# Kernel optimization log

Measured on AMD Instinct MI355X. Metric: run time of the kernel, lower is better.

## Reference

```python
import jax, jax.numpy as jnp
import numpy as np

D = 64      # feature_dim / hidden dim
L = 4       # conv layers per sub-net (len(hidden_dims))
B = 4       # query batch
N = 20000   # entity nodes
R = 256     # relation-graph nodes (= relations)
E = 300000  # entity-graph edges
ER = 40000  # edges per relation-graph direction (hh/ht/th/tt)
NNEG = 32   # candidate relations per query


def _mlp2(x, W1, b1, W2, b2):
    # Linear -> ReLU -> Linear (used for relation_projection and the 2-layer MLPs)
    return jnp.maximum(x @ W1 + b1, 0.0) @ W2 + b2


def _conv(x, boundary, rel_raw, src, dst, etype, num_nodes, W1, b1, W2, b2, Wl, bl):
    # GeneralizedRelationalConv: project relations, distmult message, sum-aggregate
    # with boundary self-loop, then linear(cat[input, agg]) + ReLU.
    rel = _mlp2(rel_raw, W1, b1, W2, b2)            # (B, R, D) relation_projection
    msg = x[:, src, :] * rel[:, etype, :]            # (B, E, D) distmult message
    agg = jax.vmap(lambda m: jax.ops.segment_sum(m, dst, num_segments=num_nodes))(msg)
    agg = agg + boundary                             # self-loop carries boundary
    out = jnp.concatenate([x, agg], axis=-1) @ Wl + bl
    return jax.nn.relu(out)


def setup_inputs() -> dict:
    key = jax.random.key(0)
    ks = jax.random.split(key, 32)
    p = lambda k, shape: jax.random.normal(k, shape, jnp.float32) * 0.05
    h = jax.random.randint(ks[0], (B,), 0, N)
    t = jax.random.randint(ks[1], (B,), 0, N)
    r = jax.random.randint(ks[2], (B, NNEG), 0, R // 2)
    batch = jnp.stack([jnp.broadcast_to(h[:, None], (B, NNEG)),
                       jnp.broadcast_to(t[:, None], (B, NNEG)), r], axis=-1)
    return {
        'batch': batch,
        'ent_edge_index': jax.random.randint(ks[3], (2, E), 0, N),
        'ent_edge_type': jax.random.randint(ks[4], (E,), 0, R),
        'rel_edge_index': jax.random.randint(ks[5], (4, 2, ER), 0, R),
        'rel_edge_type': jax.random.randint(ks[6], (4, ER), 0, N),
        'num_nodes': N,
        'num_rel_nodes': R,
        'ent_W1': p(ks[7], (L, D, D)), 'ent_b1': p(ks[8], (L, D)),
        'ent_W2': p(ks[9], (L, D, D)), 'ent_b2': p(ks[10], (L, D)),
        'ent_Wl': p(ks[11], (L, 2 * D, D)), 'ent_bl': p(ks[12], (L, D)),
        'rel_W1': p(ks[13], (4, L, D, D)), 'rel_b1': p(ks[14], (4, L, D)),
        'rel_W2': p(ks[15], (4, L, D, D)), 'rel_b2': p(ks[16], (4, L, D)),
        'rel_Wl': p(ks[17], (4, L, 2 * D, D)), 'rel_bl': p(ks[18], (4, L, D)),
        'ent_mlp_W1': p(ks[19], (2 * D, 2 * D)), 'ent_mlp_b1': p(ks[20], (2 * D,)),
        'ent_mlp_W2': p(ks[21], (2 * D, D)), 'ent_mlp_b2': p(ks[22], (D,)),
        'trix_W1': p(ks[23], (D, D)), 'trix_b1': p(ks[24], (D,)),
        'trix_W2': p(ks[25], (D, 1)), 'trix_b2': p(ks[26], (1,)),
    }


def reference(batch, ent_edge_index, ent_edge_type, rel_edge_index, rel_edge_type,
              num_nodes, num_rel_nodes,
              ent_W1, ent_b1, ent_W2, ent_b2, ent_Wl, ent_bl,
              rel_W1, rel_b1, rel_W2, rel_b2, rel_Wl, rel_bl,
              ent_mlp_W1, ent_mlp_b1, ent_mlp_W2, ent_mlp_b2,
              trix_W1, trix_b1, trix_W2, trix_b2):
    Bq = batch.shape[0]
    h, t, r = batch[:, 0, 0], batch[:, 0, 1], batch[:, :, 2]
    ar = jnp.arange(Bq)
    query = jnp.ones((Bq, D), jnp.float32)  # relation_representations start as ones
    node_reps = jnp.zeros((Bq, num_nodes, D), jnp.float32)
    node_reps = node_reps.at[ar, h].add(query).at[ar, t].add(-query)
    rel_reps = jnp.ones((Bq, num_rel_nodes, D), jnp.float32)
    esrc, edst = ent_edge_index[0], ent_edge_index[1]

    # --- TRIX block (num_layer = 1): EntityNet then RelNet ---
    # EntityNet bellman-ford over entity graph
    boundary = jnp.zeros((Bq, num_nodes, D), jnp.float32)
    boundary = boundary.at[ar, h].add(query).at[ar, t].add(-query)
    x = node_reps
    for l in range(L):
        hid = _conv(x, boundary, rel_reps, esrc, edst, ent_edge_type, num_nodes,
                    ent_W1[l], ent_b1[l], ent_W2[l], ent_b2[l], ent_Wl[l], ent_bl[l])
        x = hid + x  # short_cut
    node_query = jnp.broadcast_to(query[:, None, :], (Bq, num_nodes, D))
    feat = jnp.concatenate([x, node_query], axis=-1)  # (B, N, 2D)
    node_reps = _mlp2(feat, ent_mlp_W1, ent_mlp_b1, ent_mlp_W2, ent_mlp_b2)

    # RelNet over 4 relation-graph directions
    boundary_r = jnp.ones((Bq, num_rel_nodes, D), jnp.float32)
    y = rel_reps
    for l in range(L):
        hid = jnp.zeros_like(y)
        for d in range(4):
            hid = hid + _conv(y, boundary_r, node_reps,
                              rel_edge_index[d, 0], rel_edge_index[d, 1], rel_edge_type[d],
                              num_rel_nodes,
                              rel_W1[d, l], rel_b1[d, l], rel_W2[d, l], rel_b2[d, l],
                              rel_Wl[d, l], rel_bl[d, l])
        y = hid + y  # short_cut
    rel_reps = y

    feat = rel_reps[ar[:, None], r]  # gather candidate relation features (B, NNEG, D)
    score = _mlp2(feat, trix_W1, trix_b1, trix_W2, trix_b2)[..., 0]
    return score
```

## Files before the change

kernel.cpp:

```cpp
#include <hip/hip_runtime.h>

typedef long long i64;
#define CDIV(a,b) (((a)+(b)-1)/(b))

#define NN   20000
#define RRN  256
#define BB   4
#define LLAY 4

__global__ void k_fill2i(int* p1, int n1, int* p2, int n2){
  int i=blockIdx.x*256+threadIdx.x;
  if(i<n1) p1[i]=0;
  if(i<n2) p2[i]=0;
}

__global__ void k_hist_ent(const int* __restrict__ dst, int* __restrict__ cnt, int E){
  int e=blockIdx.x*256+threadIdx.x; if(e<E) atomicAdd(&cnt[dst[e]],1);
}
__global__ void k_scan_ent(int* cnt_cur, int* rp, int n){
  __shared__ int sm[1024];
  __shared__ int carry;
  int tx=threadIdx.x;
  if(tx==0) carry=0;
  __syncthreads();
  for(int base=0;base<n;base+=1024){
    int i=base+tx;
    int val=(i<n)?cnt_cur[i]:0;
    sm[tx]=val; __syncthreads();
    for(int off=1;off<1024;off<<=1){
      int t=(tx>=off)?sm[tx-off]:0; __syncthreads();
      sm[tx]+=t; __syncthreads();
    }
    int excl=carry+sm[tx]-val;
    if(i<n){ rp[i]=excl; cnt_cur[i]=excl; }
    __syncthreads();
    if(tx==0) carry+=sm[1023];
    __syncthreads();
  }
  if(tx==0) rp[n]=carry;
}
__global__ void k_fill_ent(const int* __restrict__ src, const int* __restrict__ dst,
                           int* __restrict__ cur, int* __restrict__ colsrc, int E){
  int e=blockIdx.x*256+threadIdx.x;
  if(e<E){ int p=atomicAdd(&cur[dst[e]],1); colsrc[p]=src[e]; }
}

__global__ void k_hist_rel(const int* __restrict__ rei, int* __restrict__ cnt, int ER){
  int e=blockIdx.x*256+threadIdx.x; int d=blockIdx.y;
  if(e<ER) atomicAdd(&cnt[d*256 + rei[(i64)(2*d+1)*ER + e]],1);
}
__global__ void k_scan_rel(int* cnt_cur, int* rp){
  __shared__ int sm[256];
  int d=blockIdx.x, tx=threadIdx.x;
  int val=cnt_cur[d*256+tx];
  sm[tx]=val; __syncthreads();
  for(int off=1;off<256;off<<=1){
    int t=(tx>=off)?sm[tx-off]:0; __syncthreads();
    sm[tx]+=t; __syncthreads();
  }
  int excl=sm[tx]-val;
  rp[d*257+tx]=excl;
  cnt_cur[d*256+tx]=excl;
  if(tx==255) rp[d*257+256]=sm[255];
}
__global__ void k_fill_rel(const int* __restrict__ rei, int* __restrict__ cur,
                           int* __restrict__ colr, int ER){
  int e=blockIdx.x*256+threadIdx.x; int d=blockIdx.y;
  if(e<ER){
    int dst=rei[(i64)(2*d+1)*ER+e];
    int p=atomicAdd(&cur[d*256+dst],1);
    colr[d*ER+p]=e;
  }
}

__global__ void k_init_x(float* __restrict__ x, const int* __restrict__ batch, int N){
  int i=blockIdx.x*256+threadIdx.x;
  int total=N*64;
  if(i>=total) return;
  int n=i>>6; int b=(i>>4)&3;
  int h=batch[b*96], t=batch[b*96+1];
  float bnd=(n==h?1.f:0.f)-(n==t?1.f:0.f);
  ((float4*)x)[i]=make_float4(bnd,bnd,bnd,bnd);
}

__global__ void k_ventity_all(const float* __restrict__ W1, const float* __restrict__ b1,
                              const float* __restrict__ W2, const float* __restrict__ b2,
                              float* __restrict__ v){
  __shared__ float sh[64];
  int l=blockIdx.x;
  const float* W1l=W1+(i64)l*4096;
  const float* W2l=W2+(i64)l*4096;
  int j=threadIdx.x;
  float s=b1[l*64+j];
  for(int i=0;i<64;i++) s+=W1l[i*64+j];
  sh[j]=fmaxf(s,0.f);
  __syncthreads();
  float vd=b2[l*64+j];
  for(int k=0;k<64;k++) vd+=sh[k]*W2l[k*64+j];
  v[l*64+j]=vd;
}

__global__ void k_badj(const float* __restrict__ W1, const float* __restrict__ b1,
                       float* __restrict__ badj){
  int j=threadIdx.x;
  float s=b1[j];
  for(int k=0;k<64;k++) s+=W1[(64+k)*128+j];
  badj[j]=s;
}

__global__ __launch_bounds__(256) void k_spmm_ent(
    const float* __restrict__ x, const float* __restrict__ v,
    const int* __restrict__ rp, const int* __restrict__ col,
    const int* __restrict__ batch, float* __restrict__ agg, int N){
  int gw=blockIdx.x*4+(threadIdx.x>>6);
  int lane=threadIdx.x&63;
  if(gw>=N) return;
  int n=gw;
  int beg=rp[n], end=rp[n+1];
  float a0=0.f,a1=0.f,a2=0.f,a3=0.f;
  int e=beg;
  for(; e+2<=end; e+=2){
    int s0=col[e], s1=col[e+1];
    const float* r0=x+(i64)s0*256;
    const float* r1=x+(i64)s1*256;
    a0+=r0[lane];     a1+=r0[64+lane];
    a2+=r0[128+lane]; a3+=r0[192+lane];
    a0+=r1[lane];     a1+=r1[64+lane];
    a2+=r1[128+lane]; a3+=r1[192+lane];
  }
  if(e<end){
    const float* r0=x+(i64)col[e]*256;
    a0+=r0[lane]; a1+=r0[64+lane]; a2+=r0[128+lane]; a3+=r0[192+lane];
  }
  float vl=v[lane];
  #pragma unroll
  for(int b=0;b<4;b++){
    int h=batch[b*96], t=batch[b*96+1];
    float bnd=(n==h?1.f:0.f)-(n==t?1.f:0.f);
    float av=(b==0)?a0:(b==1)?a1:(b==2)?a2:a3;
    agg[((i64)n*4+b)*64+lane]=av*vl+bnd;
  }
}

__global__ __launch_bounds__(256) void k_spmm_rel(
    const float* __restrict__ y, const float* __restrict__ relbuf, i64 rbs,
    const int* __restrict__ rp_rel, const int* __restrict__ col_rel,
    const int* __restrict__ rei, const int* __restrict__ ret,
    float* __restrict__ aggr, int d0, int ER){
  __shared__ float s_acc[4][4][64];
  int rr=blockIdx.x; int ch=blockIdx.y; int dz=blockIdx.z;
  int d=d0+dz;
  const float* rb=relbuf+(i64)dz*rbs;
  int tx=threadIdx.x; int ws=tx>>6; int lane=tx&63;
  int beg=rp_rel[d*257+rr], end=rp_rel[d*257+rr+1];
  int len=end-beg;
  int per=(len+3)>>2;
  int cb=beg+ch*per;
  int ce_=cb+per; if(ce_>end) ce_=end;
  int clen=ce_-cb; if(clen<0) clen=0;
  int perw=(clen+3)>>2;
  int e0=cb+ws*perw;
  int e1=e0+perw; if(e1>ce_) e1=ce_;
  const int* cidx=col_rel+(i64)d*ER;
  const int* srcA=rei+(i64)(2*d)*ER;
  const int* etA=ret+(i64)d*ER;
  float a0=0.f,a1=0.f,a2=0.f,a3=0.f;
  for(int e=e0;e<e1;++e){
    int eid=cidx[e];
    int s=srcA[eid], t=etA[eid];
    const float* yr=y+(i64)s*64;
    const float* rr2=rb+(i64)t*256;
    a0+=yr[0*16384+lane]*rr2[     lane];
    a1+=yr[1*16384+lane]*rr2[ 64+lane];
    a2+=yr[2*16384+lane]*rr2[128+lane];
    a3+=yr[3*16384+lane]*rr2[192+lane];
  }
  s_acc[ws][0][lane]=a0; s_acc[ws][1][lane]=a1;
  s_acc[ws][2][lane]=a2; s_acc[ws][3][lane]=a3;
  __syncthreads();
  int b=ws;
  float vv=s_acc[0][b][lane]+s_acc[1][b][lane]+s_acc[2][b][lane]+s_acc[3][b][lane];
  atomicAdd(&aggr[((i64)(d*4+b)*256+rr)*64+lane],vv);
}

template<int KC, bool RELU, int OP>
__global__ __launch_bounds__(256,4) void k_gemm64(
    const float* __restrict__ inA, int lda,
    const float* __restrict__ inB, int ldb, i64 inBs,
    const float* __restrict__ W, int ldw, i64 Ws,
    const float* __restrict__ bias, i64 biasS,
    float* out, int ldo, i64 outS,
    const float* resid, int ldr,
    int rows){
  __shared__ float s_in[128*68];
  __shared__ float s_wt[64*68];
  int tx=threadIdx.x;
  int dy=blockIdx.y;
  const float* Wd=W+(i64)dy*Ws;
  const float* biasd=bias+(i64)dy*biasS;
  float* outd=out+(i64)dy*outS;
  int row0=blockIdx.x*128;
  int rslot=tx>>4, c0=tx&15;
  float acc[8][4];
  #pragma unroll
  for(int j=0;j<8;j++)
    #pragma unroll
    for(int cc=0;cc<4;cc++) acc[j][cc]=0.f;
  for(int kc=0;kc<KC;++kc){
    const float* in=(kc==0)?inA:(inB+(i64)dy*inBs);
    int ld=(kc==0)?lda:ldb;
    #pragma unroll
    for(int i=0;i<8;i++){
      int id=i*256+tx;
      int r=id>>4, k4=id&15;
      int gr=row0+r;
      float4 val=make_float4(0.f,0.f,0.f,0.f);
      if(gr<rows) val=*(const float4*)(in+(i64)gr*ld+k4*4);
      *(float4*)&s_in[r*68+k4*4]=val;
    }
    #pragma unroll
    for(int i=0;i<4;i++){
      int id=i*256+tx;
      int k=id>>4, c4=(id&15)*4;
      float4 wv=*(const float4*)(Wd+(i64)(kc*64+k)*ldw+c4);
      s_wt[(c4+0)*68+k]=wv.x; s_wt[(c4+1)*68+k]=wv.y;
      s_wt[(c4+2)*68+k]=wv.z; s_wt[(c4+3)*68+k]=wv.w;
    }
    __syncthreads();
    #pragma unroll 4
    for(int k4=0;k4<16;k4++){
      float4 wv[4];
      #pragma unroll
      for(int cc=0;cc<4;cc++) wv[cc]=*(const float4*)&s_wt[(c0+16*cc)*68+k4*4];
      #pragma unroll
      for(int j=0;j<8;j++){
        float4 iv=*(const float4*)&s_in[(rslot+16*j)*68+k4*4];
        #pragma unroll
        for(int cc=0;cc<4;cc++)
          acc[j][cc]+=iv.x*wv[cc].x+iv.y*wv[cc].y+iv.z*wv[cc].z+iv.w*wv[cc].w;
      }
    }
    __syncthreads();
  }
  #pragma unroll
  for(int j=0;j<8;j++){
    int r=row0+rslot+16*j;
    if(r>=rows) continue;
    #pragma unroll
    for(int cc=0;cc<4;cc++){
      int c=c0+16*cc;
      float vv=acc[j][cc]+biasd[c];
      if(RELU) vv=fmaxf(vv,0.f);
      if(OP==1) vv+=resid[(i64)r*ldr+c];
      outd[(i64)r*ldo+c]=vv;
    }
  }
}

__global__ __launch_bounds__(256,4) void k_mlp128(
    const float* __restrict__ in,
    const float* __restrict__ W1, i64 w1s,
    const float* __restrict__ b1, i64 b1s,
    const float* __restrict__ W2, i64 w2s,
    const float* __restrict__ b2, i64 b2s,
    float* __restrict__ out, i64 outs,
    int rows){
  __shared__ float s_in[128*68];
  __shared__ float s_wt[64*68];
  int tx=threadIdx.x;
  int dy=blockIdx.y;
  const float* W1d=W1+(i64)dy*w1s;
  const float* b1d=b1+(i64)dy*b1s;
  const float* W2d=W2+(i64)dy*w2s;
  const float* b2d=b2+(i64)dy*b2s;
  float* outd=out+(i64)dy*outs;
  int row0=blockIdx.x*128;
  int rslot=tx>>4, c0=tx&15;
  #pragma unroll
  for(int i=0;i<8;i++){
    int id=i*256+tx;
    int r=id>>4, k4=id&15;
    int gr=row0+r;
    float4 val=make_float4(0.f,0.f,0.f,0.f);
    if(gr<rows) val=*(const float4*)(in+(i64)gr*64+k4*4);
    *(float4*)&s_in[r*68+k4*4]=val;
  }
  #pragma unroll
  for(int i=0;i<4;i++){
    int id=i*256+tx;
    int k=id>>4, c4=(id&15)*4;
    float4 wv=*(const float4*)(W1d+(i64)k*64+c4);
    s_wt[(c4+0)*68+k]=wv.x; s_wt[(c4+1)*68+k]=wv.y;
    s_wt[(c4+2)*68+k]=wv.z; s_wt[(c4+3)*68+k]=wv.w;
  }
  __syncthreads();
  float acc[8][4];
  #pragma unroll
  for(int j=0;j<8;j++)
    #pragma unroll
    for(int cc=0;cc<4;cc++) acc[j][cc]=0.f;
  #pragma unroll 4
  for(int k4=0;k4<16;k4++){
    float4 wv[4];
    #pragma unroll
    for(int cc=0;cc<4;cc++) wv[cc]=*(const float4*)&s_wt[(c0+16*cc)*68+k4*4];
    #pragma unroll
    for(int j=0;j<8;j++){
      float4 iv=*(const float4*)&s_in[(rslot+16*j)*68+k4*4];
      #pragma unroll
      for(int cc=0;cc<4;cc++)
        acc[j][cc]+=iv.x*wv[cc].x+iv.y*wv[cc].y+iv.z*wv[cc].z+iv.w*wv[cc].w;
    }
  }
  __syncthreads();
  #pragma unroll
  for(int j=0;j<8;j++)
    #pragma unroll
    for(int cc=0;cc<4;cc++)
      s_in[(rslot+16*j)*68+(c0+16*cc)]=fmaxf(acc[j][cc]+b1d[c0+16*cc],0.f);
  #pragma unroll
  for(int i=0;i<4;i++){
    int id=i*256+tx;
    int k=id>>4, c4=(id&15)*4;
    float4 wv=*(const float4*)(W2d+(i64)k*64+c4);
    s_wt[(c4+0)*68+k]=wv.x; s_wt[(c4+1)*68+k]=wv.y;
    s_wt[(c4+2)*68+k]=wv.z; s_wt[(c4+3)*68+k]=wv.w;
  }
  __syncthreads();
  #pragma unroll
  for(int j=0;j<8;j++)
    #pragma unroll
    for(int cc=0;cc<4;cc++) acc[j][cc]=0.f;
  #pragma unroll 4
  for(int k4=0;k4<16;k4++){
    float4 wv[4];
    #pragma unroll
    for(int cc=0;cc<4;cc++) wv[cc]=*(const float4*)&s_wt[(c0+16*cc)*68+k4*4];
    #pragma unroll
    for(int j=0;j<8;j++){
      float4 iv=*(const float4*)&s_in[(rslot+16*j)*68+k4*4];
      #pragma unroll
      for(int cc=0;cc<4;cc++)
        acc[j][cc]+=iv.x*wv[cc].x+iv.y*wv[cc].y+iv.z*wv[cc].z+iv.w*wv[cc].w;
    }
  }
  #pragma unroll
  for(int j=0;j<8;j++){
    int r=row0+rslot+16*j;
    if(r>=rows) continue;
    #pragma unroll
    for(int cc=0;cc<4;cc++)
      outd[(i64)r*64+c0+16*cc]=acc[j][cc]+b2d[c0+16*cc];
  }
}

__global__ __launch_bounds__(256,4) void k_mlp_ent(
    float* __restrict__ x,
    const float* __restrict__ W1,
    const float* __restrict__ badj,
    const float* __restrict__ W2,
    const float* __restrict__ b2o,
    int rows){
  __shared__ float s_in[64*68];
  __shared__ float s_h[64*68];
  __shared__ float s_wt[64*68];
  int tx=threadIdx.x;
  int row0=blockIdx.x*64;
  int rslot=tx>>4, c0=tx&15;
  #pragma unroll
  for(int i=0;i<4;i++){
    int id=i*256+tx;
    int r=id>>4, k4=id&15;
    int gr=row0+r;
    float4 val=make_float4(0.f,0.f,0.f,0.f);
    if(gr<rows) val=*(const float4*)(x+(i64)gr*64+k4*4);
    *(float4*)&s_in[r*68+k4*4]=val;
  }
  float accO[4][4];
  #pragma unroll
  for(int j=0;j<4;j++)
    #pragma unroll
    for(int cc=0;cc<4;cc++) accO[j][cc]=0.f;
  for(int half=0;half<2;++half){
    __syncthreads();
    #pragma unroll
    for(int i=0;i<4;i++){
      int id=i*256+tx;
      int k=id>>4, c4=(id&15)*4;
      float4 wv=*(const float4*)(W1+(i64)k*128+half*64+c4);
      s_wt[(c4+0)*68+k]=wv.x; s_wt[(c4+1)*68+k]=wv.y;
      s_wt[(c4+2)*68+k]=wv.z; s_wt[(c4+3)*68+k]=wv.w;
    }
    __syncthreads();
    float acc[4][4];
    #pragma unroll
    for(int j=0;j<4;j++)
      #pragma unroll
      for(int cc=0;cc<4;cc++) acc[j][cc]=0.f;
    #pragma unroll 4
    for(int k4=0;k4<16;k4++){
      float4 wv[4];
      #pragma unroll
      for(int cc=0;cc<4;cc++) wv[cc]=*(const float4*)&s_wt[(c0+16*cc)*68+k4*4];
      #pragma unroll
      for(int j=0;j<4;j++){
        float4 iv=*(const float4*)&s_in[(rslot+16*j)*68+k4*4];
        #pragma unroll
        for(int cc=0;cc<4;cc++)
          acc[j][cc]+=iv.x*wv[cc].x+iv.y*wv[cc].y+iv.z*wv[cc].z+iv.w*wv[cc].w;
      }
    }
    __syncthreads();
    #pragma unroll
    for(int j=0;j<4;j++)
      #pragma unroll
      for(int cc=0;cc<4;cc++)
        s_h[(rslot+16*j)*68+(c0+16*cc)]=fmaxf(acc[j][cc]+badj[half*64+c0+16*cc],0.f);
    #pragma unroll
    for(int i=0;i<4;i++){
      int id=i*256+tx;
      int k=id>>4, c4=(id&15)*4;
      float4 wv=*(const float4*)(W2+(i64)(half*64+k)*64+c4);
      s_wt[(c4+0)*68+k]=wv.x; s_wt[(c4+1)*68+k]=wv.y;
      s_wt[(c4+2)*68+k]=wv.z; s_wt[(c4+3)*68+k]=wv.w;
    }
    __syncthreads();
    #pragma unroll 4
    for(int k4=0;k4<16;k4++){
      float4 wv[4];
      #pragma unroll
      for(int cc=0;cc<4;cc++) wv[cc]=*(const float4*)&s_wt[(c0+16*cc)*68+k4*4];
      #pragma unroll
      for(int j=0;j<4;j++){
        float4 iv=*(const float4*)&s_h[(rslot+16*j)*68+k4*4];
        #pragma unroll
        for(int cc=0;cc<4;cc++)
          accO[j][cc]+=iv.x*wv[cc].x+iv.y*wv[cc].y+iv.z*wv[cc].z+iv.w*wv[cc].w;
      }
    }
  }
  #pragma unroll
  for(int j=0;j<4;j++){
    int r=row0+rslot+16*j;
    if(r>=rows) continue;
    #pragma unroll
    for(int cc=0;cc<4;cc++)
      x[(i64)r*64+c0+16*cc]=accO[j][cc]+b2o[c0+16*cc];
  }
}

__global__ void k_yupd_fill(float* __restrict__ y, const float* __restrict__ h,
                            float* __restrict__ aggr){
  int i=blockIdx.x*256+threadIdx.x;
  if(i<65536) y[i]+=h[i]+h[65536+i]+h[131072+i]+h[196608+i];
  if(i<262144) aggr[i]=1.0f;
}

__global__ void k_init_rel(float* __restrict__ y, float* __restrict__ aggr){
  int i=blockIdx.x*256+threadIdx.x;
  if(i<65536) y[i]=1.0f;
  if(i<262144) aggr[i]=1.0f;
}

__global__ __launch_bounds__(256) void k_trix(
    const float* __restrict__ y, const int* __restrict__ batch,
    const float* __restrict__ W1, const float* __restrict__ b1,
    const float* __restrict__ W2, const float* __restrict__ b2,
    float* __restrict__ out){
  __shared__ float s_w1[64*65];
  int tx=threadIdx.x;
  for(int i=tx;i<4096;i+=256){
    int k=i>>6, j=i&63;
    s_w1[k*65+j]=W1[i];
  }
  __syncthreads();
  int wave=tx>>6, lane=tx&63;
  for(int row=wave;row<128;row+=4){
    int b=row>>5, i=row&31;
    int ridx=batch[b*96+i*3+2];
    const float* f=y+((i64)b*256+ridx)*64;
    float hj=b1[lane];
    for(int k=0;k<64;k++) hj+=f[k]*s_w1[k*65+lane];
    hj=fmaxf(hj,0.f);
    float contrib=hj*W2[lane];
    for(int off=32;off;off>>=1) contrib+=__shfl_down(contrib,off);
    if(lane==0) out[row]=contrib+b2[0];
  }
}

extern "C" void kernel_launch(void* const* d_in, const int* in_sizes, int n_in,
                              void* d_out, int out_size, void* d_ws, size_t ws_size,
                              hipStream_t stream){
  const int* batch=(const int*)d_in[0];
  const int* eei  =(const int*)d_in[1];
  const int* rei  =(const int*)d_in[3];
  const int* ret  =(const int*)d_in[4];
  const float* entW1=(const float*)d_in[7];
  const float* entb1=(const float*)d_in[8];
  const float* entW2=(const float*)d_in[9];
  const float* entb2=(const float*)d_in[10];
  const float* entWl=(const float*)d_in[11];
  const float* entbl=(const float*)d_in[12];
  const float* relW1=(const float*)d_in[13];
  const float* relb1=(const float*)d_in[14];
  const float* relW2=(const float*)d_in[15];
  const float* relb2=(const float*)d_in[16];
  const float* relWl=(const float*)d_in[17];
  const float* relbl=(const float*)d_in[18];
  const float* mW1=(const float*)d_in[19];
  const float* mb1=(const float*)d_in[20];
  const float* mW2=(const float*)d_in[21];
  const float* mb2=(const float*)d_in[22];
  const float* tW1=(const float*)d_in[23];
  const float* tb1=(const float*)d_in[24];
  const float* tW2=(const float*)d_in[25];
  const float* tb2=(const float*)d_in[26];
  const int E =in_sizes[2];
  const int ER=in_sizes[4]/4;
  float* out=(float*)d_out;

  float* ws=(float*)d_ws;
  float* x     =ws;
  float* buf   =x+5120000;
  float* aggr  =buf+5120000;
  float* hidr  =aggr+262144;
  float* y     =hidr+262144;
  float* v     =y+65536;
  float* badj  =v+256;
  int* rp_ent =(int*)(badj+128);
  int* cur_ent=rp_ent+NN+1;
  int* col_ent=cur_ent+NN;
  int* rp_rel =col_ent+E;
  int* cur_rel=rp_rel+4*257;
  int* col_rel=cur_rel+1024;
  size_t buf2_off=((size_t)(col_rel+4*ER-(int*)d_ws)+3)&~(size_t)3;
  float* buf2 =(float*)d_ws+buf2_off;

  size_t needed =(buf2_off)*4;
  size_t needed2=(buf2_off+(size_t)5120000)*4;
  if(ws_size<needed) return;
  const bool two=(ws_size>=needed2);
  const i64 bufStride=(i64)(buf2-buf);

  const int* esrc=eei;
  const int* edst=eei+E;

  k_fill2i<<<CDIV(NN,256),256,0,stream>>>(cur_ent,NN,cur_rel,1024);
  k_hist_ent<<<CDIV(E,256),256,0,stream>>>(edst,cur_ent,E);
  k_scan_ent<<<1,1024,0,stream>>>(cur_ent,rp_ent,NN);
  k_fill_ent<<<CDIV(E,256),256,0,stream>>>(esrc,edst,cur_ent,col_ent,E);
  k_hist_rel<<<dim3(CDIV(ER,256),4),256,0,stream>>>(rei,cur_rel,ER);
  k_scan_rel<<<4,256,0,stream>>>(cur_rel,rp_rel);
  k_fill_rel<<<dim3(CDIV(ER,256),4),256,0,stream>>>(rei,cur_rel,col_rel,ER);

  k_ventity_all<<<LLAY,64,0,stream>>>(entW1,entb1,entW2,entb2,v);
  k_badj<<<1,128,0,stream>>>(mW1,mb1,badj);

  k_init_x<<<CDIV(NN*64,256),256,0,stream>>>(x,batch,NN);
  for(int l=0;l<LLAY;l++){
    k_spmm_ent<<<CDIV(NN,4),256,0,stream>>>(x,v+(i64)l*64,rp_ent,col_ent,batch,buf,NN);
    k_gemm64<2,true,1><<<625,256,0,stream>>>(x,64, buf,64,0,
        entWl+(i64)l*8192,64,0, entbl+(i64)l*64,0, x,64,0, x,64, 80000);
  }
  k_mlp_ent<<<1250,256,0,stream>>>(x,mW1,badj,mW2,mb2,80000);

  k_init_rel<<<1024,256,0,stream>>>(y,aggr);
  for(int l=0;l<LLAY;l++){
    if(two){
      for(int d=0;d<4;d+=2){
        k_mlp128<<<dim3(625,2),256,0,stream>>>(x,
            relW1+(i64)(d*LLAY+l)*4096,(i64)LLAY*4096,
            relb1+(i64)(d*LLAY+l)*64,(i64)LLAY*64,
            relW2+(i64)(d*LLAY+l)*4096,(i64)LLAY*4096,
            relb2+(i64)(d*LLAY+l)*64,(i64)LLAY*64,
            buf,bufStride, 80000);
        k_spmm_rel<<<dim3(256,4,2),256,0,stream>>>(y,buf,bufStride,
            rp_rel,col_rel,rei,ret,aggr,d,ER);
      }
    } else {
      for(int d=0;d<4;d++){
        k_mlp128<<<dim3(625,1),256,0,stream>>>(x,
            relW1+(i64)(d*LLAY+l)*4096,0,
            relb1+(i64)(d*LLAY+l)*64,0,
            relW2+(i64)(d*LLAY+l)*4096,0,
            relb2+(i64)(d*LLAY+l)*64,0,
            buf,0, 80000);
        k_spmm_rel<<<dim3(256,4,1),256,0,stream>>>(y,buf,0,
            rp_rel,col_rel,rei,ret,aggr,d,ER);
      }
    }
    k_gemm64<2,true,0><<<dim3(8,4),256,0,stream>>>(y,64, aggr,64,(i64)65536,
        relWl+(i64)l*8192,64,(i64)LLAY*8192, relbl+(i64)l*64,(i64)LLAY*64,
        hidr,64,(i64)65536, y,64, 1024);
    k_yupd_fill<<<1024,256,0,stream>>>(y,hidr,aggr);
  }

  k_trix<<<1,256,0,stream>>>(y,batch,tW1,tb1,tW2,tb2,out);
}
```

Measured before the change: 1.324 ms.

## Vectorize SpMM kernels, drop atomics and batch all four relation directions

The entity SpMM now has each lane load a float4 of the 4x64 row and unrolls edges by four. The relation SpMM gives each relation node a single block per direction, reduces across waves in shared memory and writes the result with the +1 boundary folded in. That removes the atomicAdd and the separate aggr fill kernel. Workspace is now sized to hold up to four relation-projection buffers, so k_mlp128 and k_spmm_rel can cover all four directions in one launch when memory allows. The trade-offs are less parallelism per relation node in spmm_rel (no edge chunking across blocks) and a larger workspace requirement for the batched path.

```diff
diff --git a/kernel.cpp b/kernel.cpp
--- a/kernel.cpp
+++ b/kernel.cpp
@@ -8,6 +8,7 @@
 #define BB   4
 #define LLAY 4
 
+__global__ void k_fillf(float* p, float v, int n){ int i=blockIdx.x*256+threadIdx.x; if(i<n) p[i]=v; }
 __global__ void k_fill2i(int* p1, int n1, int* p2, int n2){
   int i=blockIdx.x*256+threadIdx.x;
   if(i<n1) p1[i]=0;
@@ -112,34 +113,34 @@
     const float* __restrict__ x, const float* __restrict__ v,
     const int* __restrict__ rp, const int* __restrict__ col,
     const int* __restrict__ batch, float* __restrict__ agg, int N){
-  int gw=blockIdx.x*4+(threadIdx.x>>6);
+  int n=blockIdx.x*4+(threadIdx.x>>6);
   int lane=threadIdx.x&63;
-  if(gw>=N) return;
-  int n=gw;
+  if(n>=N) return;
   int beg=rp[n], end=rp[n+1];
-  float a0=0.f,a1=0.f,a2=0.f,a3=0.f;
+  float4 a=make_float4(0.f,0.f,0.f,0.f);
   int e=beg;
-  for(; e+2<=end; e+=2){
-    int s0=col[e], s1=col[e+1];
-    const float* r0=x+(i64)s0*256;
-    const float* r1=x+(i64)s1*256;
-    a0+=r0[lane];     a1+=r0[64+lane];
-    a2+=r0[128+lane]; a3+=r0[192+lane];
-    a0+=r1[lane];     a1+=r1[64+lane];
-    a2+=r1[128+lane]; a3+=r1[192+lane];
-  }
-  if(e<end){
-    const float* r0=x+(i64)col[e]*256;
-    a0+=r0[lane]; a1+=r0[64+lane]; a2+=r0[128+lane]; a3+=r0[192+lane];
-  }
-  float vl=v[lane];
-  #pragma unroll
-  for(int b=0;b<4;b++){
-    int h=batch[b*96], t=batch[b*96+1];
-    float bnd=(n==h?1.f:0.f)-(n==t?1.f:0.f);
-    float av=(b==0)?a0:(b==1)?a1:(b==2)?a2:a3;
-    agg[((i64)n*4+b)*64+lane]=av*vl+bnd;
-  }
+  for(; e+4<=end; e+=4){
+    int s0=col[e], s1=col[e+1], s2=col[e+2], s3=col[e+3];
+    float4 r0=*(const float4*)&x[(i64)s0*256+lane*4];
+    float4 r1=*(const float4*)&x[(i64)s1*256+lane*4];
+    float4 r2=*(const float4*)&x[(i64)s2*256+lane*4];
+    float4 r3=*(const float4*)&x[(i64)s3*256+lane*4];
+    a.x+=r0.x+r1.x+r2.x+r3.x;
+    a.y+=r0.y+r1.y+r2.y+r3.y;
+    a.z+=r0.z+r1.z+r2.z+r3.z;
+    a.w+=r0.w+r1.w+r2.w+r3.w;
+  }
+  for(; e<end; ++e){
+    float4 r0=*(const float4*)&x[(i64)col[e]*256+lane*4];
+    a.x+=r0.x; a.y+=r0.y; a.z+=r0.z; a.w+=r0.w;
+  }
+  int b=lane>>4;
+  float4 v4=*(const float4*)&v[(lane&15)*4];
+  int h=batch[b*96], t=batch[b*96+1];
+  float bnd=(n==h?1.f:0.f)-(n==t?1.f:0.f);
+  float4 o;
+  o.x=a.x*v4.x+bnd; o.y=a.y*v4.y+bnd; o.z=a.z*v4.z+bnd; o.w=a.w*v4.w+bnd;
+  *(float4*)&agg[(i64)n*256+lane*4]=o;
 }
 
 __global__ __launch_bounds__(256) void k_spmm_rel(
@@ -147,40 +148,52 @@
     const int* __restrict__ rp_rel, const int* __restrict__ col_rel,
     const int* __restrict__ rei, const int* __restrict__ ret,
     float* __restrict__ aggr, int d0, int ER){
-  __shared__ float s_acc[4][4][64];
-  int rr=blockIdx.x; int ch=blockIdx.y; int dz=blockIdx.z;
-  int d=d0+dz;
+  __shared__ float4 s_acc[4][64];
+  int rr=blockIdx.x; int dz=blockIdx.y; int d=d0+dz;
   const float* rb=relbuf+(i64)dz*rbs;
-  int tx=threadIdx.x; int ws=tx>>6; int lane=tx&63;
+  int tx=threadIdx.x; int wsl=tx>>6; int lane=tx&63;
   int beg=rp_rel[d*257+rr], end=rp_rel[d*257+rr+1];
   int len=end-beg;
-  int per=(len+3)>>2;
-  int cb=beg+ch*per;
-  int ce_=cb+per; if(ce_>end) ce_=end;
-  int clen=ce_-cb; if(clen<0) clen=0;
-  int perw=(clen+3)>>2;
-  int e0=cb+ws*perw;
-  int e1=e0+perw; if(e1>ce_) e1=ce_;
+  int perw=(len+3)>>2;
+  int e0=beg+wsl*perw;
+  int e1=e0+perw; if(e1>end) e1=end;
   const int* cidx=col_rel+(i64)d*ER;
   const int* srcA=rei+(i64)(2*d)*ER;
   const int* etA=ret+(i64)d*ER;
-  float a0=0.f,a1=0.f,a2=0.f,a3=0.f;
-  for(int e=e0;e<e1;++e){
-    int eid=cidx[e];
-    int s=srcA[eid], t=etA[eid];
-    const float* yr=y+(i64)s*64;
-    const float* rr2=rb+(i64)t*256;
-    a0+=yr[0*16384+lane]*rr2[     lane];
-    a1+=yr[1*16384+lane]*rr2[ 64+lane];
-    a2+=yr[2*16384+lane]*rr2[128+lane];
-    a3+=yr[3*16384+lane]*rr2[192+lane];
-  }
-  s_acc[ws][0][lane]=a0; s_acc[ws][1][lane]=a1;
-  s_acc[ws][2][lane]=a2; s_acc[ws][3][lane]=a3;
-  __syncthreads();
-  int b=ws;
-  float vv=s_acc[0][b][lane]+s_acc[1][b][lane]+s_acc[2][b][lane]+s_acc[3][b][lane];
-  atomicAdd(&aggr[((i64)(d*4+b)*256+rr)*64+lane],vv);
+  int b=lane>>4; int ch4=(lane&15)*4;
+  float4 a=make_float4(0.f,0.f,0.f,0.f);
+  int e=e0;
+  for(; e+2<=e1; e+=2){
+    int eA=cidx[e], eB=cidx[e+1];
+    int sA=srcA[eA], tA=etA[eA];
+    int sB=srcA[eB], tB=etA[eB];
+    float4 yA=*(const float4*)&y[(i64)b*16384+(i64)sA*64+ch4];
+    float4 rA=*(const float4*)&rb[(i64)tA*256+lane*4];
+    float4 yB=*(const float4*)&y[(i64)b*16384+(i64)sB*64+ch4];
+    float4 rB=*(const float4*)&rb[(i64)tB*256+lane*4];
+    a.x+=yA.x*rA.x+yB.x*rB.x;
+    a.y+=yA.y*rA.y+yB.y*rB.y;
+    a.z+=yA.z*rA.z+yB.z*rB.z;
+    a.w+=yA.w*rA.w+yB.w*rB.w;
+  }
+  if(e<e1){
+    int eA=cidx[e];
+    int sA=srcA[eA], tA=etA[eA];
+    float4 yA=*(const float4*)&y[(i64)b*16384+(i64)sA*64+ch4];
+    float4 rA=*(const float4*)&rb[(i64)tA*256+lane*4];
+    a.x+=yA.x*rA.x; a.y+=yA.y*rA.y; a.z+=yA.z*rA.z; a.w+=yA.w*rA.w;
+  }
+  s_acc[wsl][lane]=a;
+  __syncthreads();
+  if(wsl==0){
+    float4 p0=s_acc[0][lane], p1=s_acc[1][lane], p2=s_acc[2][lane], p3=s_acc[3][lane];
+    float4 o;
+    o.x=1.0f+p0.x+p1.x+p2.x+p3.x;
+    o.y=1.0f+p0.y+p1.y+p2.y+p3.y;
+    o.z=1.0f+p0.z+p1.z+p2.z+p3.z;
+    o.w=1.0f+p0.w+p1.w+p2.w+p3.w;
+    *(float4*)&aggr[((i64)(d*4+b)*256+rr)*64+ch4]=o;
+  }
 }
 
 template<int KC, bool RELU, int OP>
@@ -449,17 +462,9 @@
   }
 }
 
-__global__ void k_yupd_fill(float* __restrict__ y, const float* __restrict__ h,
-                            float* __restrict__ aggr){
+__global__ void k_yupdate4(float* __restrict__ y, const float* __restrict__ h, int n){
   int i=blockIdx.x*256+threadIdx.x;
-  if(i<65536) y[i]+=h[i]+h[65536+i]+h[131072+i]+h[196608+i];
-  if(i<262144) aggr[i]=1.0f;
-}
-
-__global__ void k_init_rel(float* __restrict__ y, float* __restrict__ aggr){
-  int i=blockIdx.x*256+threadIdx.x;
-  if(i<65536) y[i]=1.0f;
-  if(i<262144) aggr[i]=1.0f;
+  if(i<n) y[i]+=h[i]+h[(i64)n+i]+h[(i64)2*n+i]+h[(i64)3*n+i];
 }
 
 __global__ __launch_bounds__(256) void k_trix(
@@ -521,8 +526,7 @@
 
   float* ws=(float*)d_ws;
   float* x     =ws;
-  float* buf   =x+5120000;
-  float* aggr  =buf+5120000;
+  float* aggr  =x+5120000;
   float* hidr  =aggr+262144;
   float* y     =hidr+262144;
   float* v     =y+65536;
@@ -533,14 +537,13 @@
   int* rp_rel =col_ent+E;
   int* cur_rel=rp_rel+4*257;
   int* col_rel=cur_rel+1024;
-  size_t buf2_off=((size_t)(col_rel+4*ER-(int*)d_ws)+3)&~(size_t)3;
-  float* buf2 =(float*)d_ws+buf2_off;
-
-  size_t needed =(buf2_off)*4;
-  size_t needed2=(buf2_off+(size_t)5120000)*4;
-  if(ws_size<needed) return;
-  const bool two=(ws_size>=needed2);
-  const i64 bufStride=(i64)(buf2-buf);
+  size_t base_words=((size_t)(col_rel+4*ER-(int*)d_ws)+3)&~(size_t)3;
+  float* bufR=(float*)d_ws+base_words;
+  size_t avail=(ws_size/4>base_words)?(ws_size/4-base_words):0;
+  const int nb = avail>=(size_t)4*5120000 ? 4 : avail>=(size_t)2*5120000 ? 2 :
+                 avail>=(size_t)5120000 ? 1 : 0;
+  if(nb==0) return;
+  const i64 BSTRIDE=5120000;
 
   const int* esrc=eei;
   const int* edst=eei+E;
@@ -558,41 +561,29 @@
 
   k_init_x<<<CDIV(NN*64,256),256,0,stream>>>(x,batch,NN);
   for(int l=0;l<LLAY;l++){
-    k_spmm_ent<<<CDIV(NN,4),256,0,stream>>>(x,v+(i64)l*64,rp_ent,col_ent,batch,buf,NN);
-    k_gemm64<2,true,1><<<625,256,0,stream>>>(x,64, buf,64,0,
+    k_spmm_ent<<<CDIV(NN,4),256,0,stream>>>(x,v+(i64)l*64,rp_ent,col_ent,batch,bufR,NN);
+    k_gemm64<2,true,1><<<625,256,0,stream>>>(x,64, bufR,64,0,
         entWl+(i64)l*8192,64,0, entbl+(i64)l*64,0, x,64,0, x,64, 80000);
   }
   k_mlp_ent<<<1250,256,0,stream>>>(x,mW1,badj,mW2,mb2,80000);
 
-  k_init_rel<<<1024,256,0,stream>>>(y,aggr);
+  k_fillf<<<256,256,0,stream>>>(y,1.0f,65536);
   for(int l=0;l<LLAY;l++){
-    if(two){
-      for(int d=0;d<4;d+=2){
-        k_mlp128<<<dim3(625,2),256,0,stream>>>(x,
-            relW1+(i64)(d*LLAY+l)*4096,(i64)LLAY*4096,
-            relb1+(i64)(d*LLAY+l)*64,(i64)LLAY*64,
-            relW2+(i64)(d*LLAY+l)*4096,(i64)LLAY*4096,
-            relb2+(i64)(d*LLAY+l)*64,(i64)LLAY*64,
-            buf,bufStride, 80000);
-        k_spmm_rel<<<dim3(256,4,2),256,0,stream>>>(y,buf,bufStride,
-            rp_rel,col_rel,rei,ret,aggr,d,ER);
-      }
-    } else {
-      for(int d=0;d<4;d++){
-        k_mlp128<<<dim3(625,1),256,0,stream>>>(x,
-            relW1+(i64)(d*LLAY+l)*4096,0,
-            relb1+(i64)(d*LLAY+l)*64,0,
-            relW2+(i64)(d*LLAY+l)*4096,0,
-            relb2+(i64)(d*LLAY+l)*64,0,
-            buf,0, 80000);
-        k_spmm_rel<<<dim3(256,4,1),256,0,stream>>>(y,buf,0,
-            rp_rel,col_rel,rei,ret,aggr,d,ER);
-      }
+    for(int d0=0;d0<4;d0+=nb){
+      int nd=(4-d0<nb)?(4-d0):nb;
+      k_mlp128<<<dim3(625,nd),256,0,stream>>>(x,
+          relW1+(i64)(d0*LLAY+l)*4096,(i64)LLAY*4096,
+          relb1+(i64)(d0*LLAY+l)*64,(i64)LLAY*64,
+          relW2+(i64)(d0*LLAY+l)*4096,(i64)LLAY*4096,
+          relb2+(i64)(d0*LLAY+l)*64,(i64)LLAY*64,
+          bufR,BSTRIDE, 80000);
+      k_spmm_rel<<<dim3(256,nd),256,0,stream>>>(y,bufR,BSTRIDE,
+          rp_rel,col_rel,rei,ret,aggr,d0,ER);
     }
     k_gemm64<2,true,0><<<dim3(8,4),256,0,stream>>>(y,64, aggr,64,(i64)65536,
         relWl+(i64)l*8192,64,(i64)LLAY*8192, relbl+(i64)l*64,(i64)LLAY*64,
         hidr,64,(i64)65536, y,64, 1024);
-    k_yupd_fill<<<1024,256,0,stream>>>(y,hidr,aggr);
+    k_yupdate4<<<256,256,0,stream>>>(y,hidr,65536);
   }
 
   k_trix<<<1,256,0,stream>>>(y,batch,tW1,tb1,tW2,tb2,out);
```

After: 1.262 ms. -4.7%, faster.
